# Optimization experiments

Measured on AMD Instinct MI355X. Metric: run time of the kernel, lower is better.

The kernel has to match this reference:

```python
import jax, jax.numpy as jnp
import numpy as np

N = 100000      # nodes
E = 3200000     # edges (before self loops)
IN, H, OUT = 512, 256, 64
K = 10
TEMP = 1.5
EPS = 1e-5


def setup_inputs() -> dict:
    key = jax.random.key(0)
    ks = jax.random.split(key, 16)
    def lin(k, fan_in, fan_out):
        lim = 1.0 / np.sqrt(fan_in)
        kw, kb = jax.random.split(k)
        w = jax.random.uniform(kw, (fan_in, fan_out), jnp.float32, -lim, lim)
        b = jax.random.uniform(kb, (fan_out,), jnp.float32, -lim, lim)
        return w, b
    w1, b1 = lin(ks[0], IN, H)
    w2, b2 = lin(ks[1], H, H)
    w3, b3 = lin(ks[2], H, H)
    w4, b4 = lin(ks[3], H, OUT)
    return {
        "x": jax.random.normal(ks[4], (N, IN), jnp.float32),
        "edge_index": jax.random.randint(ks[5], (2, E), 0, N, jnp.int64),
        "w1": w1, "b1": b1, "g1": jnp.ones((H,), jnp.float32), "be1": jnp.zeros((H,), jnp.float32),
        "w2": w2, "b2": b2, "g2": jnp.ones((H,), jnp.float32), "be2": jnp.zeros((H,), jnp.float32),
        "w3": w3, "b3": b3, "g3": jnp.ones((H,), jnp.float32), "be3": jnp.zeros((H,), jnp.float32),
        "w4": w4, "b4": b4,
        "alpha": jnp.full((K + 1,), 1.0 / (K + 1), jnp.float32),
    }


def _bn(h, g, b):
    # batch-statistics BatchNorm1d (training-mode normalization, biased var)
    m = h.mean(axis=0)
    v = ((h - m) ** 2).mean(axis=0)
    return g * (h - m) * jax.lax.rsqrt(v + EPS) + b


def reference(x, edge_index, w1, b1, g1, be1, w2, b2, g2, be2,
              w3, b3, g3, be3, w4, b4, alpha):
    n = x.shape[0]
    # add self loops
    loop = jnp.arange(n, dtype=edge_index.dtype)
    row = jnp.concatenate([edge_index[0], loop])
    col = jnp.concatenate([edge_index[1], loop])
    # symmetric normalization D^{-1/2} A D^{-1/2} (degree counted on row)
    deg = jax.ops.segment_sum(jnp.ones_like(row, x.dtype), row, num_segments=n)
    dinv = jnp.where(deg > 0, jax.lax.rsqrt(deg), 0.0)
    norm = dinv[row] * dinv[col]  # [E+N]

    gelu = lambda h: jax.nn.gelu(h, approximate=False)
    x0 = gelu(_bn(x @ w1 + b1, g1, be1))
    x1 = gelu(_bn(x0 @ w2 + b2, g2, be2) + x0)   # dropout=identity (eval)
    x2 = gelu(_bn(x1 @ w3 + b3, g3, be3) + x1)
    h = x2 @ w4 + b4                              # [N, OUT]

    def step(carry, a):
        xt, acc = carry
        xt = jax.ops.segment_sum(norm[:, None] * xt[col], row, num_segments=n)
        return (xt, acc + a * xt), None

    (_, acc), _ = jax.lax.scan(step, (h, alpha[0] * h), alpha[1:])
    return acc / TEMP
```

## Files before the change

### kernel.cpp

```cpp
#include <hip/hip_runtime.h>
#include <math.h>

#define N_NODES 100000
#define N_IN 512
#define N_H 256
#define N_OUT 64
#define KHOP 10
#define EPS_BN 1e-5f
#define INV_TEMP (1.0f/1.5f)

using half8  = __attribute__((ext_vector_type(8))) _Float16;
using half4  = __attribute__((ext_vector_type(4))) _Float16;
using floatx4 = __attribute__((ext_vector_type(4))) float;

struct ZPtrs { const _Float16* p[KHOP]; };


__global__ void init_kernel(int* __restrict__ cnt, int n) {
    int i = blockIdx.x * blockDim.x + threadIdx.x;
    if (i < n) cnt[i] = 0;
}

__global__ __launch_bounds__(256) void fused_pre_kernel(
    const int* __restrict__ ei, int* __restrict__ cnt, unsigned short* __restrict__ pos,
    const float* __restrict__ x, _Float16* __restrict__ xh,
    const float* __restrict__ w1, _Float16* __restrict__ w1T,
    const float* __restrict__ w2, _Float16* __restrict__ w2T,
    const float* __restrict__ w3, _Float16* __restrict__ w3T,
    const float* __restrict__ w4, _Float16* __restrict__ w4T,
    int E, int nbE, int x4, int nbX4) {
    int bid = blockIdx.x;
    int t = threadIdx.x;
    if (bid < nbE) {
        int i = bid * 256 + t;
        if (i < E) {
            int r = ei[i];
            pos[i] = (unsigned short)atomicAdd(&cnt[r], 1);
        }
        return;
    }
    bid -= nbE;
    if (bid < nbX4) {
        int i = bid * 256 + t;
        if (i < x4) {
            float4 v = reinterpret_cast<const float4*>(x)[i];
            half4 h;
            h.x = (_Float16)v.x; h.y = (_Float16)v.y; h.z = (_Float16)v.z; h.w = (_Float16)v.w;
            reinterpret_cast<half4*>(xh)[i] = h;
        }
        return;
    }
    bid -= nbX4;
    if (bid < 512) {
        int i = bid * 256 + t;
        int k = i >> 8, n = i & 255;
        w1T[(size_t)n * 512 + k] = (_Float16)w1[i];
        return;
    }
    bid -= 512;
    if (bid < 256) {
        int i = bid * 256 + t;
        int k = i >> 8, n = i & 255;
        w2T[(size_t)n * 256 + k] = (_Float16)w2[i];
        return;
    }
    bid -= 256;
    if (bid < 256) {
        int i = bid * 256 + t;
        int k = i >> 8, n = i & 255;
        w3T[(size_t)n * 256 + k] = (_Float16)w3[i];
        return;
    }
    bid -= 256;
    {
        int i = bid * 256 + t;
        int k = i >> 6, n = i & 63;
        w4T[(size_t)n * 256 + k] = (_Float16)w4[i];
    }
}

__global__ void scan1_kernel(const int* __restrict__ cnt, int* __restrict__ excl,
                             int* __restrict__ bsum, int n) {
    __shared__ int sd[256];
    int t = threadIdx.x;
    int base = blockIdx.x * 1024 + t * 4;
    int v0 = (base + 0 < n) ? cnt[base + 0] + 1 : 0;
    int v1 = (base + 1 < n) ? cnt[base + 1] + 1 : 0;
    int v2 = (base + 2 < n) ? cnt[base + 2] + 1 : 0;
    int v3 = (base + 3 < n) ? cnt[base + 3] + 1 : 0;
    int tot = v0 + v1 + v2 + v3;
    sd[t] = tot;
    __syncthreads();
    for (int off = 1; off < 256; off <<= 1) {
        int x = (t >= off) ? sd[t - off] : 0;
        __syncthreads();
        sd[t] += x;
        __syncthreads();
    }
    int run = sd[t] - tot;
    if (t == 255) bsum[blockIdx.x] = sd[t];
    if (base + 0 < n) excl[base + 0] = run; run += v0;
    if (base + 1 < n) excl[base + 1] = run; run += v1;
    if (base + 2 < n) excl[base + 2] = run; run += v2;
    if (base + 3 < n) excl[base + 3] = run;
}

__global__ void scan2_kernel(int* __restrict__ bsum, int nb) {
    __shared__ int sd[128];
    int t = threadIdx.x;
    int v = (t < nb) ? bsum[t] : 0;
    sd[t] = v;
    __syncthreads();
    for (int off = 1; off < 128; off <<= 1) {
        int x = (t >= off) ? sd[t - off] : 0;
        __syncthreads();
        sd[t] += x;
        __syncthreads();
    }
    if (t < nb) bsum[t] = sd[t] - v;
}

__global__ void scan3_kernel(int* __restrict__ row_ptr, const int* __restrict__ bsum,
                             const int* __restrict__ cnt, float* __restrict__ dinv,
                             float* __restrict__ dinv2, float* __restrict__ sqd,
                             int* __restrict__ colv, int n, int total) {
    int i = blockIdx.x * blockDim.x + threadIdx.x;
    if (i < n) {
        int rp = row_ptr[i] + bsum[i >> 10];
        row_ptr[i] = rp;
        int cv = cnt[i];
        float d = (float)(cv + 1);
        dinv[i]  = rsqrtf(d);
        dinv2[i] = 1.0f / d;
        sqd[i]   = sqrtf(d);
        colv[rp + cv] = i;
    }
    if (i == 0) row_ptr[n] = total;
}

__global__ void fill_kernel(const int* __restrict__ ei, const unsigned short* __restrict__ pos,
                            const int* __restrict__ row_ptr,
                            int* __restrict__ colv, int E, int r0, int r1) {
    int i = blockIdx.x * blockDim.x + threadIdx.x;
    if (i >= E) return;
    int r = ei[i];
    if (r < r0 || r >= r1) return;
    colv[row_ptr[r] + pos[i]] = ei[E + i];
}


template<int KDIM, int NDIM, int BN, bool STATS, bool WRITE_Z, typename CT>
__global__ __launch_bounds__(256) void gemm_mfma_kernel(
    const _Float16* __restrict__ A, const _Float16* __restrict__ BT,
    const float* __restrict__ bias, CT* __restrict__ C, int M,
    float* __restrict__ sums, const float* __restrict__ dinv,
    _Float16* __restrict__ z0) {
    constexpr int BM = 128;
    constexpr int LDK = 40;
    constexpr int WTN = BN / 32;
    __shared__ _Float16 As[BM * LDK];
    __shared__ _Float16 Bs[BN * LDK];
    __shared__ float cs[BN];
    __shared__ float cq[BN];
    int t = threadIdx.x;
    int mbase = blockIdx.y * BM;
    int nbase = blockIdx.x * BN;
    int wv = t >> 6, lane = t & 63;
    int wm = (wv & 1) * 64;
    int wn = (wv >> 1) * (BN / 2);
    int q = lane >> 4;
    int fr = lane & 15;
    int sr = t >> 2;
    int sc = (t & 3) * 8;

    floatx4 acc[4][WTN];
    for (int mt = 0; mt < 4; ++mt)
        for (int nt = 0; nt < WTN; ++nt)
            acc[mt][nt] = floatx4{0.f, 0.f, 0.f, 0.f};

    for (int k0 = 0; k0 < KDIM; k0 += 32) {
        #pragma unroll
        for (int p = 0; p < 2; ++p) {
            int row = sr + p * 64;
            int grow = mbase + row;
            half8 v = {};
            if (grow < M)
                v = *reinterpret_cast<const half8*>(&A[(size_t)grow * KDIM + k0 + sc]);
            *reinterpret_cast<half8*>(&As[row * LDK + sc]) = v;
        }
        #pragma unroll
        for (int p = 0; p < BN / 64; ++p) {
            int row = sr + p * 64;
            half8 v = *reinterpret_cast<const half8*>(&BT[(size_t)(nbase + row) * KDIM + k0 + sc]);
            *reinterpret_cast<half8*>(&Bs[row * LDK + sc]) = v;
        }
        __syncthreads();
        half8 af[4], bf[WTN];
        #pragma unroll
        for (int mt = 0; mt < 4; ++mt)
            af[mt] = *reinterpret_cast<const half8*>(&As[(wm + mt * 16 + fr) * LDK + q * 8]);
        #pragma unroll
        for (int nt = 0; nt < WTN; ++nt)
            bf[nt] = *reinterpret_cast<const half8*>(&Bs[(wn + nt * 16 + fr) * LDK + q * 8]);
        #pragma unroll
        for (int mt = 0; mt < 4; ++mt)
            #pragma unroll
            for (int nt = 0; nt < WTN; ++nt)
                acc[mt][nt] = __builtin_amdgcn_mfma_f32_16x16x32_f16(af[mt], bf[nt], acc[mt][nt], 0, 0, 0);
        __syncthreads();
    }
    if constexpr (STATS) {
        if (t < BN) { cs[t] = 0.f; cq[t] = 0.f; }
        __syncthreads();
    }
    #pragma unroll
    for (int nt = 0; nt < WTN; ++nt) {
        int col = nbase + wn + nt * 16 + fr;
        float bv = bias[col];
        float s = 0.f, s2 = 0.f;
        #pragma unroll
        for (int mt = 0; mt < 4; ++mt) {
            #pragma unroll
            for (int rr = 0; rr < 4; ++rr) {
                int row = mbase + wm + mt * 16 + q * 4 + rr;
                if (row < M) {
                    float v = acc[mt][nt][rr] + bv;
                    C[(size_t)row * NDIM + col] = (CT)v;
                    if constexpr (STATS) { s += v; s2 += v * v; }
                    if constexpr (WRITE_Z)
                        z0[((size_t)row << 6) + col] = (_Float16)(dinv[row] * v);
                }
            }
        }
        if constexpr (STATS) {
            s  += __shfl_xor(s, 16);  s  += __shfl_xor(s, 32);
            s2 += __shfl_xor(s2, 16); s2 += __shfl_xor(s2, 32);
            if (q == 0) {
                atomicAdd(&cs[wn + nt * 16 + fr], s);
                atomicAdd(&cq[wn + nt * 16 + fr], s2);
            }
        }
    }
    if constexpr (STATS) {
        __syncthreads();
        if (t < BN) {
            atomicAdd(&sums[nbase + t], cs[t]);
            atomicAdd(&sums[N_H + nbase + t], cq[t]);
        }
    }
}


__global__ void finalize_stats_kernel(const float* __restrict__ sums,
                                      const float* __restrict__ g, const float* __restrict__ be,
                                      float* __restrict__ ab, float invM) {
    int c = threadIdx.x;
    float mean = sums[c] * invM;
    float var = sums[N_H + c] * invM - mean * mean;
    float a = g[c] * rsqrtf(var + EPS_BN);
    ab[c] = a;
    ab[N_H + c] = be[c] - mean * a;
}

__global__ void bn_gelu_kernel(const _Float16* __restrict__ T, const float* __restrict__ ab,
                               const _Float16* __restrict__ res, _Float16* __restrict__ Y,
                               int total4) {
    int i = blockIdx.x * blockDim.x + threadIdx.x;
    if (i >= total4) return;
    int c0 = (i * 4) & (N_H - 1);
    half4 tv = reinterpret_cast<const half4*>(T)[i];
    float4 av = *reinterpret_cast<const float4*>(&ab[c0]);
    float4 bv = *reinterpret_cast<const float4*>(&ab[N_H + c0]);
    float v0 = av.x * (float)tv.x + bv.x;
    float v1 = av.y * (float)tv.y + bv.y;
    float v2 = av.z * (float)tv.z + bv.z;
    float v3 = av.w * (float)tv.w + bv.w;
    if (res) {
        half4 rv = reinterpret_cast<const half4*>(res)[i];
        v0 += (float)rv.x; v1 += (float)rv.y; v2 += (float)rv.z; v3 += (float)rv.w;
    }
    half4 o;
    o.x = (_Float16)(0.5f * v0 * (1.f + erff(v0 * 0.70710678118654752f)));
    o.y = (_Float16)(0.5f * v1 * (1.f + erff(v1 * 0.70710678118654752f)));
    o.z = (_Float16)(0.5f * v2 * (1.f + erff(v2 * 0.70710678118654752f)));
    o.w = (_Float16)(0.5f * v3 * (1.f + erff(v3 * 0.70710678118654752f)));
    reinterpret_cast<half4*>(Y)[i] = o;
}


__global__ __launch_bounds__(256) void prop_kernel(
    const _Float16* __restrict__ zin, _Float16* __restrict__ zout,
    const int* __restrict__ colv, const int* __restrict__ row_ptr,
    const float* __restrict__ dinv2, int n) {
    int r = (blockIdx.x << 2) + (threadIdx.x >> 6);
    if (r >= n) return;
    int lane = threadIdx.x & 63;
    int esub = lane >> 4;
    int fo = (lane & 15) << 2;
    int s = __builtin_amdgcn_readfirstlane(row_ptr[r]);
    int e = __builtin_amdgcn_readfirstlane(row_ptr[r + 1]);
    float a0 = 0.f, a1 = 0.f, a2 = 0.f, a3 = 0.f;
    int i = s;
    for (; i + 16 <= e; i += 16) {
        int c0 = colv[i + esub];
        int c1 = colv[i + 4 + esub];
        int c2 = colv[i + 8 + esub];
        int c3 = colv[i + 12 + esub];
        half4 v0 = *reinterpret_cast<const half4*>(&zin[((size_t)c0 << 6) + fo]);
        half4 v1 = *reinterpret_cast<const half4*>(&zin[((size_t)c1 << 6) + fo]);
        half4 v2 = *reinterpret_cast<const half4*>(&zin[((size_t)c2 << 6) + fo]);
        half4 v3 = *reinterpret_cast<const half4*>(&zin[((size_t)c3 << 6) + fo]);
        a0 += (float)v0.x + (float)v1.x + (float)v2.x + (float)v3.x;
        a1 += (float)v0.y + (float)v1.y + (float)v2.y + (float)v3.y;
        a2 += (float)v0.z + (float)v1.z + (float)v2.z + (float)v3.z;
        a3 += (float)v0.w + (float)v1.w + (float)v2.w + (float)v3.w;
    }
    for (; i + 4 <= e; i += 4) {
        int c = colv[i + esub];
        half4 v = *reinterpret_cast<const half4*>(&zin[((size_t)c << 6) + fo]);
        a0 += (float)v.x; a1 += (float)v.y; a2 += (float)v.z; a3 += (float)v.w;
    }
    int rem = e - i;
    if (esub < rem) {
        int c = colv[i + esub];
        half4 v = *reinterpret_cast<const half4*>(&zin[((size_t)c << 6) + fo]);
        a0 += (float)v.x; a1 += (float)v.y; a2 += (float)v.z; a3 += (float)v.w;
    }
    a0 += __shfl_xor(a0, 16); a1 += __shfl_xor(a1, 16);
    a2 += __shfl_xor(a2, 16); a3 += __shfl_xor(a3, 16);
    a0 += __shfl_xor(a0, 32); a1 += __shfl_xor(a1, 32);
    a2 += __shfl_xor(a2, 32); a3 += __shfl_xor(a3, 32);
    if (lane < 16) {
        float d = dinv2[r];
        half4 o;
        o.x = (_Float16)(a0 * d); o.y = (_Float16)(a1 * d);
        o.z = (_Float16)(a2 * d); o.w = (_Float16)(a3 * d);
        *reinterpret_cast<half4*>(&zout[((size_t)r << 6) + fo]) = o;
    }
}

__global__ void prop_final_kernel(const float* __restrict__ h, ZPtrs zp,
                                  const float* __restrict__ sqd,
                                  const float* __restrict__ alpha,
                                  float* __restrict__ out, int total4) {
    int i = blockIdx.x * blockDim.x + threadIdx.x;
    if (i >= total4) return;
    int r = i >> 4;
    float4 hv = reinterpret_cast<const float4*>(h)[i];
    float s0 = 0.f, s1 = 0.f, s2 = 0.f, s3 = 0.f;
    #pragma unroll
    for (int k = 0; k < KHOP; ++k) {
        half4 z = reinterpret_cast<const half4*>(zp.p[k])[i];
        float ak = alpha[k + 1];
        s0 += ak * (float)z.x; s1 += ak * (float)z.y;
        s2 += ak * (float)z.z; s3 += ak * (float)z.w;
    }
    float sq = sqd[r];
    float a0 = alpha[0];
    float4 o;
    o.x = INV_TEMP * (a0 * hv.x + sq * s0);
    o.y = INV_TEMP * (a0 * hv.y + sq * s1);
    o.z = INV_TEMP * (a0 * hv.z + sq * s2);
    o.w = INV_TEMP * (a0 * hv.w + sq * s3);
    reinterpret_cast<float4*>(out)[i] = o;
}


extern "C" void kernel_launch(void* const* d_in, const int* in_sizes, int n_in,
                              void* d_out, int out_size, void* d_ws, size_t ws_size,
                              hipStream_t stream) {
    const float* x    = (const float*)d_in[0];
    const int*   ei   = (const int*)d_in[1];
    const float* w1   = (const float*)d_in[2];
    const float* b1   = (const float*)d_in[3];
    const float* g1   = (const float*)d_in[4];
    const float* be1  = (const float*)d_in[5];
    const float* w2   = (const float*)d_in[6];
    const float* b2   = (const float*)d_in[7];
    const float* g2   = (const float*)d_in[8];
    const float* be2  = (const float*)d_in[9];
    const float* w3   = (const float*)d_in[10];
    const float* b3   = (const float*)d_in[11];
    const float* g3   = (const float*)d_in[12];
    const float* be3  = (const float*)d_in[13];
    const float* w4   = (const float*)d_in[14];
    const float* b4   = (const float*)d_in[15];
    const float* alpha= (const float*)d_in[16];
    float* out = (float*)d_out;

    const int N = in_sizes[0] / N_IN;
    const int E = in_sizes[1] / 2;
    const int EN = E + N;
    const size_t NZ = (size_t)N * N_OUT;

    char* ws = (char*)d_ws;
    size_t off = 0;
    auto alloc = [&](size_t bytes) -> void* {
        void* p = ws + off;
        off = (off + bytes + 255) & ~(size_t)255;
        return p;
    };
    int*   cnt     = (int*)alloc((size_t)N * 4);
    int*   row_ptr = (int*)alloc((size_t)(N + 1) * 4);
    float* dinv    = (float*)alloc((size_t)N * 4);
    float* dinv2   = (float*)alloc((size_t)N * 4);
    float* sqd     = (float*)alloc((size_t)N * 4);
    int*   colv    = (int*)alloc((size_t)EN * 4);
    unsigned short* pos = (unsigned short*)alloc((size_t)E * 2);
    int*   bsum    = (int*)alloc(128 * 4);
    float* sums    = (float*)alloc(2 * N_H * 4);
    float* ab      = (float*)alloc(2 * N_H * 4);
    _Float16* w1T  = (_Float16*)alloc((size_t)N_IN * N_H * 2);
    _Float16* w2T  = (_Float16*)alloc((size_t)N_H * N_H * 2);
    _Float16* w3T  = (_Float16*)alloc((size_t)N_H * N_H * 2);
    _Float16* w4T  = (_Float16*)alloc((size_t)N_H * N_OUT * 2);
    _Float16* xh   = (_Float16*)alloc((size_t)N * N_IN * 2);
    float* T       = (float*)alloc((size_t)N * N_H * 4);
    _Float16* Ah0  = (_Float16*)alloc((size_t)N * N_H * 2);
    _Float16* Ah1  = (_Float16*)alloc((size_t)N * N_H * 2);
    float* hbuf    = (float*)alloc((size_t)N * N_OUT * 4);
    _Float16* z0   = (_Float16*)alloc(NZ * 2);

    _Float16* Tf16 = (_Float16*)T;

    _Float16* zk[KHOP + 1];
    zk[0] = z0;
    for (int k = 1; k <= 8; ++k) zk[k] = (_Float16*)T + (size_t)(k - 1) * NZ;
    zk[9]  = (_Float16*)Ah1;
    zk[10] = (_Float16*)Ah1 + NZ;

    const int TB = 256;
    int nbN  = (N + TB - 1) / TB;
    int nbE  = (E + TB - 1) / TB;
    int nscan = (N + 1023) / 1024;
    int x4 = N * N_IN / 4;
    int nbX4 = (x4 + TB - 1) / TB;

    init_kernel<<<nbN, TB, 0, stream>>>(cnt, N);
    {
        int grid = nbE + nbX4 + 512 + 256 + 256 + 64;
        fused_pre_kernel<<<grid, TB, 0, stream>>>(ei, cnt, pos, x, xh,
                                                  w1, w1T, w2, w2T, w3, w3T, w4, w4T,
                                                  E, nbE, x4, nbX4);
    }

    scan1_kernel<<<nscan, TB, 0, stream>>>(cnt, row_ptr, bsum, N);
    scan2_kernel<<<1, 128, 0, stream>>>(bsum, nscan);
    scan3_kernel<<<nbN, TB, 0, stream>>>(row_ptr, bsum, cnt, dinv, dinv2, sqd, colv, N, EN);

    {
        const int P = 4;
        int step = (N + P - 1) / P;
        for (int p = 0; p < P; ++p) {
            int r0 = p * step;
            int r1 = min(N, r0 + step);
            fill_kernel<<<nbE, TB, 0, stream>>>(ei, pos, row_ptr, colv, E, r0, r1);
        }
    }

    int mt = (N + 127) / 128;
    int elemH4 = N * N_H / 4;
    int nbElemH4 = (elemH4 + TB - 1) / TB;

    hipMemsetAsync(sums, 0, 2 * N_H * 4, stream);
    gemm_mfma_kernel<N_IN, N_H, 128, true, false, _Float16><<<dim3(N_H / 128, mt), TB, 0, stream>>>(
        xh, w1T, b1, Tf16, N, sums, nullptr, nullptr);
    finalize_stats_kernel<<<1, N_H, 0, stream>>>(sums, g1, be1, ab, 1.0f / N);
    bn_gelu_kernel<<<nbElemH4, TB, 0, stream>>>(Tf16, ab, nullptr, Ah0, elemH4);
    hipMemsetAsync(sums, 0, 2 * N_H * 4, stream);
    gemm_mfma_kernel<N_H, N_H, 128, true, false, _Float16><<<dim3(N_H / 128, mt), TB, 0, stream>>>(
        Ah0, w2T, b2, Tf16, N, sums, nullptr, nullptr);
    finalize_stats_kernel<<<1, N_H, 0, stream>>>(sums, g2, be2, ab, 1.0f / N);
    bn_gelu_kernel<<<nbElemH4, TB, 0, stream>>>(Tf16, ab, Ah0, Ah1, elemH4);
    hipMemsetAsync(sums, 0, 2 * N_H * 4, stream);
    gemm_mfma_kernel<N_H, N_H, 128, true, false, _Float16><<<dim3(N_H / 128, mt), TB, 0, stream>>>(
        Ah1, w3T, b3, Tf16, N, sums, nullptr, nullptr);
    finalize_stats_kernel<<<1, N_H, 0, stream>>>(sums, g3, be3, ab, 1.0f / N);
    bn_gelu_kernel<<<nbElemH4, TB, 0, stream>>>(Tf16, ab, Ah1, Ah0, elemH4);
    gemm_mfma_kernel<N_H, N_OUT, 64, false, true, float><<<dim3(1, mt), TB, 0, stream>>>(
        Ah0, w4T, b4, hbuf, N, nullptr, dinv, z0);

    int nbProp = (N + 3) / 4;
    for (int k = 1; k <= KHOP; ++k) {
        prop_kernel<<<nbProp, TB, 0, stream>>>(zk[k - 1], zk[k], colv, row_ptr, dinv2, N);
    }

    ZPtrs zp;
    for (int k = 0; k < KHOP; ++k) zp.p[k] = zk[k + 1];
    int total4 = N * N_OUT / 4;
    prop_final_kernel<<<(total4 + TB - 1) / TB, TB, 0, stream>>>(hbuf, zp, sqd, alpha, out, total4);
}
```

Measured before the change: 1.522 ms.

## Fuse BatchNorm+GELU and fp16 input conversion into GEMM A-tile loads

The standalone bn_gelu kernels and the x fp32-to-fp16 conversion pass are removed. Each GEMM now applies the previous layer's BN affine, residual and GELU while loading its A tile, and writes the activation out for later residual use. The first GEMM converts fp32 x on the fly. GEMMs use a full-width 256-column tile so each row block is processed once, which avoids recomputing GELU and allows Tf16 to be overwritten in place. Stats zeroing moves into init/finalize, replacing the memsets. This cuts several full passes over large activation buffers, at the cost of more registers and ALU work inside the GEMM load path.

Measured after the change: 1.732 ms. 13.8% more time.

```diff
diff --git a/kernel.cpp b/kernel.cpp
--- a/kernel.cpp
+++ b/kernel.cpp
@@ -16,19 +16,19 @@
 struct ZPtrs { const _Float16* p[KHOP]; };
 
 
-__global__ void init_kernel(int* __restrict__ cnt, int n) {
+__global__ void init_kernel(int* __restrict__ cnt, float* __restrict__ sums, int n) {
     int i = blockIdx.x * blockDim.x + threadIdx.x;
     if (i < n) cnt[i] = 0;
+    if (i < 2 * N_H) sums[i] = 0.f;
 }
 
 __global__ __launch_bounds__(256) void fused_pre_kernel(
     const int* __restrict__ ei, int* __restrict__ cnt, unsigned short* __restrict__ pos,
-    const float* __restrict__ x, _Float16* __restrict__ xh,
     const float* __restrict__ w1, _Float16* __restrict__ w1T,
     const float* __restrict__ w2, _Float16* __restrict__ w2T,
     const float* __restrict__ w3, _Float16* __restrict__ w3T,
     const float* __restrict__ w4, _Float16* __restrict__ w4T,
-    int E, int nbE, int x4, int nbX4) {
+    int E, int nbE) {
     int bid = blockIdx.x;
     int t = threadIdx.x;
     if (bid < nbE) {
@@ -40,17 +40,6 @@
         return;
     }
     bid -= nbE;
-    if (bid < nbX4) {
-        int i = bid * 256 + t;
-        if (i < x4) {
-            float4 v = reinterpret_cast<const float4*>(x)[i];
-            half4 h;
-            h.x = (_Float16)v.x; h.y = (_Float16)v.y; h.z = (_Float16)v.z; h.w = (_Float16)v.w;
-            reinterpret_cast<half4*>(xh)[i] = h;
-        }
-        return;
-    }
-    bid -= nbX4;
     if (bid < 512) {
         int i = bid * 256 + t;
         int k = i >> 8, n = i & 255;
@@ -149,12 +138,15 @@
 }
 
 
-template<int KDIM, int NDIM, int BN, bool STATS, bool WRITE_Z, typename CT>
+#define GELU(u) (0.5f * (u) * (1.f + erff((u) * 0.70710678118654752f)))
+
+template<int KDIM, int NDIM, int BN, int AMODE, bool STATS, bool WRITE_X, bool WRITE_Z, typename CT>
 __global__ __launch_bounds__(256) void gemm_mfma_kernel(
-    const _Float16* __restrict__ A, const _Float16* __restrict__ BT,
+    const void* __restrict__ Araw, const _Float16* __restrict__ BT,
     const float* __restrict__ bias, CT* __restrict__ C, int M,
-    float* __restrict__ sums, const float* __restrict__ dinv,
-    _Float16* __restrict__ z0) {
+    float* __restrict__ sums, const float* __restrict__ ab,
+    const _Float16* __restrict__ res, _Float16* __restrict__ xout,
+    const float* __restrict__ dinv, _Float16* __restrict__ z0) {
     constexpr int BM = 128;
     constexpr int LDK = 40;
     constexpr int WTN = BN / 32;
@@ -179,19 +171,58 @@
             acc[mt][nt] = floatx4{0.f, 0.f, 0.f, 0.f};
 
     for (int k0 = 0; k0 < KDIM; k0 += 32) {
+        int kc = k0 + sc;
         #pragma unroll
         for (int p = 0; p < 2; ++p) {
             int row = sr + p * 64;
             int grow = mbase + row;
             half8 v = {};
-            if (grow < M)
-                v = *reinterpret_cast<const half8*>(&A[(size_t)grow * KDIM + k0 + sc]);
+            if (grow < M) {
+                if constexpr (AMODE == 0) {
+                    v = *reinterpret_cast<const half8*>(
+                        &((const _Float16*)Araw)[(size_t)grow * KDIM + kc]);
+                } else if constexpr (AMODE == 1) {
+                    const float* Af = (const float*)Araw + (size_t)grow * KDIM + kc;
+                    float4 f0 = *reinterpret_cast<const float4*>(Af);
+                    float4 f1 = *reinterpret_cast<const float4*>(Af + 4);
+                    v[0] = (_Float16)f0.x; v[1] = (_Float16)f0.y;
+                    v[2] = (_Float16)f0.z; v[3] = (_Float16)f0.w;
+                    v[4] = (_Float16)f1.x; v[5] = (_Float16)f1.y;
+                    v[6] = (_Float16)f1.z; v[7] = (_Float16)f1.w;
+                } else {
+                    half8 tv = *reinterpret_cast<const half8*>(
+                        &((const _Float16*)Araw)[(size_t)grow * KDIM + kc]);
+                    float4 a0 = *reinterpret_cast<const float4*>(&ab[kc]);
+                    float4 a1 = *reinterpret_cast<const float4*>(&ab[kc + 4]);
+                    float4 b0 = *reinterpret_cast<const float4*>(&ab[KDIM + kc]);
+                    float4 b1 = *reinterpret_cast<const float4*>(&ab[KDIM + kc + 4]);
+                    float u[8];
+                    u[0] = a0.x * (float)tv[0] + b0.x;
+                    u[1] = a0.y * (float)tv[1] + b0.y;
+                    u[2] = a0.z * (float)tv[2] + b0.z;
+                    u[3] = a0.w * (float)tv[3] + b0.w;
+                    u[4] = a1.x * (float)tv[4] + b1.x;
+                    u[5] = a1.y * (float)tv[5] + b1.y;
+                    u[6] = a1.z * (float)tv[6] + b1.z;
+                    u[7] = a1.w * (float)tv[7] + b1.w;
+                    if constexpr (AMODE == 3) {
+                        half8 rv = *reinterpret_cast<const half8*>(
+                            &res[(size_t)grow * KDIM + kc]);
+                        #pragma unroll
+                        for (int j = 0; j < 8; ++j) u[j] += (float)rv[j];
+                    }
+                    #pragma unroll
+                    for (int j = 0; j < 8; ++j) v[j] = (_Float16)GELU(u[j]);
+                    if constexpr (WRITE_X)
+                        *reinterpret_cast<half8*>(&xout[(size_t)grow * KDIM + kc]) = v;
+                }
+            }
             *reinterpret_cast<half8*>(&As[row * LDK + sc]) = v;
         }
         #pragma unroll
         for (int p = 0; p < BN / 64; ++p) {
             int row = sr + p * 64;
-            half8 v = *reinterpret_cast<const half8*>(&BT[(size_t)(nbase + row) * KDIM + k0 + sc]);
+            half8 v = *reinterpret_cast<const half8*>(&BT[(size_t)(nbase + row) * KDIM + kc]);
             *reinterpret_cast<half8*>(&Bs[row * LDK + sc]) = v;
         }
         __syncthreads();
@@ -251,40 +282,18 @@
 }
 
 
-__global__ void finalize_stats_kernel(const float* __restrict__ sums,
+__global__ void finalize_stats_kernel(float* __restrict__ sums,
                                       const float* __restrict__ g, const float* __restrict__ be,
                                       float* __restrict__ ab, float invM) {
     int c = threadIdx.x;
-    float mean = sums[c] * invM;
-    float var = sums[N_H + c] * invM - mean * mean;
+    float s = sums[c], s2 = sums[N_H + c];
+    float mean = s * invM;
+    float var = s2 * invM - mean * mean;
     float a = g[c] * rsqrtf(var + EPS_BN);
     ab[c] = a;
     ab[N_H + c] = be[c] - mean * a;
-}
-
-__global__ void bn_gelu_kernel(const _Float16* __restrict__ T, const float* __restrict__ ab,
-                               const _Float16* __restrict__ res, _Float16* __restrict__ Y,
-                               int total4) {
-    int i = blockIdx.x * blockDim.x + threadIdx.x;
-    if (i >= total4) return;
-    int c0 = (i * 4) & (N_H - 1);
-    half4 tv = reinterpret_cast<const half4*>(T)[i];
-    float4 av = *reinterpret_cast<const float4*>(&ab[c0]);
-    float4 bv = *reinterpret_cast<const float4*>(&ab[N_H + c0]);
-    float v0 = av.x * (float)tv.x + bv.x;
-    float v1 = av.y * (float)tv.y + bv.y;
-    float v2 = av.z * (float)tv.z + bv.z;
-    float v3 = av.w * (float)tv.w + bv.w;
-    if (res) {
-        half4 rv = reinterpret_cast<const half4*>(res)[i];
-        v0 += (float)rv.x; v1 += (float)rv.y; v2 += (float)rv.z; v3 += (float)rv.w;
-    }
-    half4 o;
-    o.x = (_Float16)(0.5f * v0 * (1.f + erff(v0 * 0.70710678118654752f)));
-    o.y = (_Float16)(0.5f * v1 * (1.f + erff(v1 * 0.70710678118654752f)));
-    o.z = (_Float16)(0.5f * v2 * (1.f + erff(v2 * 0.70710678118654752f)));
-    o.w = (_Float16)(0.5f * v3 * (1.f + erff(v3 * 0.70710678118654752f)));
-    reinterpret_cast<half4*>(Y)[i] = o;
+    sums[c] = 0.f;
+    sums[N_H + c] = 0.f;
 }
 
 
@@ -414,7 +423,6 @@
     _Float16* w2T  = (_Float16*)alloc((size_t)N_H * N_H * 2);
     _Float16* w3T  = (_Float16*)alloc((size_t)N_H * N_H * 2);
     _Float16* w4T  = (_Float16*)alloc((size_t)N_H * N_OUT * 2);
-    _Float16* xh   = (_Float16*)alloc((size_t)N * N_IN * 2);
     float* T       = (float*)alloc((size_t)N * N_H * 4);
     _Float16* Ah0  = (_Float16*)alloc((size_t)N * N_H * 2);
     _Float16* Ah1  = (_Float16*)alloc((size_t)N * N_H * 2);
@@ -433,15 +441,13 @@
     int nbN  = (N + TB - 1) / TB;
     int nbE  = (E + TB - 1) / TB;
     int nscan = (N + 1023) / 1024;
-    int x4 = N * N_IN / 4;
-    int nbX4 = (x4 + TB - 1) / TB;
-
-    init_kernel<<<nbN, TB, 0, stream>>>(cnt, N);
+
+    init_kernel<<<nbN, TB, 0, stream>>>(cnt, sums, N);
     {
-        int grid = nbE + nbX4 + 512 + 256 + 256 + 64;
-        fused_pre_kernel<<<grid, TB, 0, stream>>>(ei, cnt, pos, x, xh,
+        int grid = nbE + 512 + 256 + 256 + 64;
+        fused_pre_kernel<<<grid, TB, 0, stream>>>(ei, cnt, pos,
                                                   w1, w1T, w2, w2T, w3, w3T, w4, w4T,
-                                                  E, nbE, x4, nbX4);
+                                                  E, nbE);
     }
 
     scan1_kernel<<<nscan, TB, 0, stream>>>(cnt, row_ptr, bsum, N);
@@ -459,26 +465,22 @@
     }
 
     int mt = (N + 127) / 128;
-    int elemH4 = N * N_H / 4;
-    int nbElemH4 = (elemH4 + TB - 1) / TB;
-
-    hipMemsetAsync(sums, 0, 2 * N_H * 4, stream);
-    gemm_mfma_kernel<N_IN, N_H, 128, true, false, _Float16><<<dim3(N_H / 128, mt), TB, 0, stream>>>(
-        xh, w1T, b1, Tf16, N, sums, nullptr, nullptr);
+
+    gemm_mfma_kernel<N_IN, N_H, 256, 1, true, false, false, _Float16>
+        <<<dim3(1, mt), TB, 0, stream>>>(
+        x, w1T, b1, Tf16, N, sums, nullptr, nullptr, nullptr, nullptr, nullptr);
     finalize_stats_kernel<<<1, N_H, 0, stream>>>(sums, g1, be1, ab, 1.0f / N);
-    bn_gelu_kernel<<<nbElemH4, TB, 0, stream>>>(Tf16, ab, nullptr, Ah0, elemH4);
-    hipMemsetAsync(sums, 0, 2 * N_H * 4, stream);
-    gemm_mfma_kernel<N_H, N_H, 128, true, false, _Float16><<<dim3(N_H / 128, mt), TB, 0, stream>>>(
-        Ah0, w2T, b2, Tf16, N, sums, nullptr, nullptr);
+    gemm_mfma_kernel<N_H, N_H, 256, 2, true, true, false, _Float16>
+        <<<dim3(1, mt), TB, 0, stream>>>(
+        Tf16, w2T, b2, Tf16, N, sums, ab, nullptr, Ah0, nullptr, nullptr);
     finalize_stats_kernel<<<1, N_H, 0, stream>>>(sums, g2, be2, ab, 1.0f / N);
-    bn_gelu_kernel<<<nbElemH4, TB, 0, stream>>>(Tf16, ab, Ah0, Ah1, elemH4);
-    hipMemsetAsync(sums, 0, 2 * N_H * 4, stream);
-    gemm_mfma_kernel<N_H, N_H, 128, true, false, _Float16><<<dim3(N_H / 128, mt), TB, 0, stream>>>(
-        Ah1, w3T, b3, Tf16, N, sums, nullptr, nullptr);
+    gemm_mfma_kernel<N_H, N_H, 256, 3, true, true, false, _Float16>
+        <<<dim3(1, mt), TB, 0, stream>>>(
+        Tf16, w3T, b3, Tf16, N, sums, ab, Ah0, Ah1, nullptr, nullptr);
     finalize_stats_kernel<<<1, N_H, 0, stream>>>(sums, g3, be3, ab, 1.0f / N);
-    bn_gelu_kernel<<<nbElemH4, TB, 0, stream>>>(Tf16, ab, Ah1, Ah0, elemH4);
-    gemm_mfma_kernel<N_H, N_OUT, 64, false, true, float><<<dim3(1, mt), TB, 0, stream>>>(
-        Ah0, w4T, b4, hbuf, N, nullptr, dinv, z0);
+    gemm_mfma_kernel<N_H, N_OUT, 64, 3, false, false, true, float>
+        <<<dim3(1, mt), TB, 0, stream>>>(
+        Tf16, w4T, b4, hbuf, N, nullptr, ab, Ah1, nullptr, dinv, z0);
 
     int nbProp = (N + 3) / 4;
     for (int k = 1; k <= KHOP; ++k) {
```
